# Performance work log

Measured on AMD Instinct MI355X. Metric: run time of the kernel, lower is better.

The kernel has to match this reference:

```python
import jax, jax.numpy as jnp
import numpy as np

NUM_HEADS = 8
CHUNK = 64          # dialtion / chunck_size
EPS = 1e-5          # InstanceNorm1d eps
NEG = -1e9


def setup_inputs() -> dict:
    key = jax.random.key(0)
    ks = jax.random.split(key, 8)
    N, C, T = 4, 512, 4096
    x = jax.random.normal(ks[0], (N, C, T), dtype=jnp.float32)
    q = jax.random.normal(ks[1], (N, C, T), dtype=jnp.float32)
    k = jax.random.normal(ks[2], (N, C, T), dtype=jnp.float32)
    v = jax.random.normal(ks[3], (N, C, T), dtype=jnp.float32)
    masks = jnp.ones((N, 1, T), dtype=jnp.float32)
    s = 1.0 / np.sqrt(C)
    W_in = jax.random.normal(ks[4], (3 * C, C), dtype=jnp.float32) * s   # packed q/k/v in-proj
    b_in = jnp.zeros((3 * C,), dtype=jnp.float32)
    W_out = jax.random.normal(ks[5], (C, C), dtype=jnp.float32) * s     # out-proj
    b_out = jnp.zeros((C,), dtype=jnp.float32)
    return {"x": x, "q": q, "k": k, "v": v, "masks": masks,
            "W_in": W_in, "b_in": b_in, "W_out": W_out, "b_out": b_out}


def _chunk_attn(q, k, v, masks, W_in, b_in, W_out, b_out):
    # q,k,v: [N, C, T]; masks: [N, 1, T]
    N, C, T = q.shape
    H, Dh = NUM_HEADS, C // NUM_HEADS
    nc = T // CHUNK
    Wq, Wk, Wv = jnp.split(W_in, 3, axis=0)
    bq, bk, bv = jnp.split(b_in, 3, axis=0)

    def proj(t, W, b):
        # [N,C,T] -> chunked heads [N, nc, CHUNK, H, Dh]
        t = t.transpose(0, 2, 1) @ W.T + b            # [N, T, C]
        return t.reshape(N, nc, CHUNK, H, Dh)

    qh = proj(q, Wq, bq)
    kh = proj(k, Wk, bk)
    vh = proj(v, Wv, bv)

    scale = 1.0 / jnp.sqrt(jnp.asarray(Dh, q.dtype))
    # intra-chunk scores: [N, nc, H, CHUNK, CHUNK]
    scores = jnp.einsum('bnqhd,bnkhd->bnhqk', qh, kh) * scale
    km = masks[:, 0, :].reshape(N, nc, CHUNK)         # key validity per chunk
    scores = scores + jnp.where(km[:, :, None, None, :] > 0, 0.0, NEG)
    attn = jax.nn.softmax(scores, axis=-1)
    out = jnp.einsum('bnhqk,bnkhd->bnqhd', attn, vh).reshape(N, T, C)
    out = out @ W_out.T + b_out                        # [N, T, C]
    out = out.transpose(0, 2, 1) * masks               # [N, C, T], re-mask
    return out


def reference(x, q, k, v, masks, W_in, b_in, W_out, b_out):
    out = _chunk_attn(q, k, v, masks, W_in, b_in, W_out, b_out) + x
    # InstanceNorm1d (affine=False): normalize each (n, c) row over T
    mu = jnp.mean(out, axis=2, keepdims=True)
    var = jnp.mean(jnp.square(out - mu), axis=2, keepdims=True)
    return (out - mu) * jax.lax.rsqrt(var + EPS)
```

## Files before the change

### kernel.cpp

```cpp
#include <hip/hip_runtime.h>
#include <hip/hip_bf16.h>

#define NB 4
#define CC 512
#define TT 4096
#define C3 1536
#define CQK 1024
#define NTC (NB*TT*CC)

typedef __attribute__((ext_vector_type(4))) float f32x4;
typedef __attribute__((ext_vector_type(8))) short short8;
typedef unsigned short ushort;
typedef __attribute__((ext_vector_type(8))) ushort u16x8;

__device__ __forceinline__ ushort f2bf(float f){
    union { float f; unsigned u; } x; x.f = f;
    unsigned r = x.u + 0x7fffu + ((x.u >> 16) & 1u);
    return (ushort)(r >> 16);
}

__device__ __forceinline__ ushort2 pk2bf(float a, float b){
    float2 f2; f2.x = a; f2.y = b;
    __hip_bfloat162 h = __float22bfloat162_rn(f2);
    union { __hip_bfloat162 h2; ushort2 u2; } u; u.h2 = h;
    return u.u2;
}

__device__ __forceinline__ void gload16(const void* g, void* l){
    __builtin_amdgcn_global_load_lds((const __attribute__((address_space(1))) void*)g,
                                     (__attribute__((address_space(3))) void*)l,
                                     16, 0, 0);
}

__device__ __forceinline__ int apos(int m, int cb){
    return (m*8 + ((cb + m + (m >> 3)) & 7))*8;
}

__global__ __launch_bounds__(256) void wcvt(const float* __restrict__ Wi,
                                            const float* __restrict__ Wo,
                                            ushort* __restrict__ Wb,
                                            ushort* __restrict__ Wob){
    int idx0 = blockIdx.x * 1024 + threadIdx.x;
    for (int i = 0; i < 4; ++i){
        int idx = idx0 + i*256;
        const float* src; ushort* dst; int j;
        if (idx < 196608){ src = Wi; dst = Wb;  j = idx; }
        else             { src = Wo; dst = Wob; j = idx - 196608; }
        f32x4 vv = *((const f32x4*)src + j);
        ushort4 o;
        *(ushort2*)&o.x = pk2bf(vv[0], vv[1]);
        *(ushort2*)&o.z = pk2bf(vv[2], vv[3]);
        *((ushort4*)dst + j) = o;
    }
}

__global__ __launch_bounds__(256, 3) void proj_gemm(const float* __restrict__ q,
                                                    const float* __restrict__ k,
                                                    const float* __restrict__ v,
                                                    const ushort* __restrict__ Wb,
                                                    const float* __restrict__ b_in,
                                                    ushort* __restrict__ P,
                                                    ushort* __restrict__ Vt){
    __shared__ __align__(16) ushort smem[24576];
    ushort* sA  = smem;
    ushort* sB0 = smem + 8192;
    ushort* sB1 = smem + 16384;
    const int tid = threadIdx.x;
    const int bid = blockIdx.x;
    const int mtile  = ((bid & 7) << 4) | ((bid >> 3) & 15);
    const int cotile = bid >> 7;
    const int co0 = cotile * 128;
    const int m0  = mtile * 128;
    const int which = co0 >> 9;
    const float* src = (which == 0) ? q : (which == 1) ? k : v;
    const int n  = m0 >> 12, t0 = m0 & 4095;
    const ushort* Bbase = Wb + (size_t)co0*CC;
    const int w = tid >> 6, lane = tid & 63;
    const int wr = w >> 1, wc = w & 1;
    const int l15 = lane & 15, quad = lane >> 4;
    const int hlf = lane >> 5, tq = lane & 31;

    const int mrB = tid >> 3;
    const int kkB = (tid & 7) ^ (mrB & 7);
    const ushort* gB0 = Bbase + (size_t)mrB*CC + kkB*8;
    const int lB0 = (tid & ~63) * 8;

    const float* Ab = src + (size_t)n*CC*TT + t0 + tq*4;
    const int ce0 = w*16 + hlf*2;

    f32x4 a0[4], a1[4];
    #pragma unroll
    for (int u = 0; u < 4; ++u){
        a0[u] = *(const f32x4*)(Ab + (size_t)(ce0 + u*4    )*TT);
        a1[u] = *(const f32x4*)(Ab + (size_t)(ce0 + u*4 + 1)*TT);
    }
    #pragma unroll
    for (int i = 0; i < 4; ++i)
        gload16(gB0 + (size_t)i*32*CC, sB0 + lB0 + i*2048);
    #pragma unroll
    for (int u = 0; u < 4; ++u){
        int ce = ce0 + u*4;
        int cb = ce >> 3, off = ce & 7;
        #pragma unroll
        for (int j = 0; j < 4; ++j)
            *(ushort2*)&sA[apos(tq*4 + j, cb) + off] = pk2bf(a0[u][j], a1[u][j]);
    }
    __syncthreads();

    f32x4 acc[4][4] = {};
    for (int kb = 0; kb < 8; ++kb){
        ushort* sBc = (kb & 1) ? sB1 : sB0;
        ushort* sBn = (kb & 1) ? sB0 : sB1;
        if (kb < 7){
            const float* Abn = Ab + (size_t)((kb+1)*64)*TT;
            #pragma unroll
            for (int u = 0; u < 4; ++u){
                a0[u] = *(const f32x4*)(Abn + (size_t)(ce0 + u*4    )*TT);
                a1[u] = *(const f32x4*)(Abn + (size_t)(ce0 + u*4 + 1)*TT);
            }
            #pragma unroll
            for (int i = 0; i < 4; ++i)
                gload16(gB0 + (size_t)i*32*CC + (kb+1)*64, sBn + lB0 + i*2048);
        }
        #pragma unroll
        for (int ks = 0; ks < 2; ++ks){
            short8 aF[4], bF[4];
            #pragma unroll
            for (int mi = 0; mi < 4; ++mi){
                int m = wr*64 + mi*16 + l15;
                aF[mi] = *(const short8*)&sA[apos(m, ks*4 + quad)];
            }
            #pragma unroll
            for (int ni = 0; ni < 4; ++ni){
                int m = wc*64 + ni*16 + l15;
                bF[ni] = *(const short8*)&sBc[(m*8 + ((ks*4 + quad) ^ (m & 7)))*8];
            }
            #pragma unroll
            for (int mi = 0; mi < 4; ++mi)
                #pragma unroll
                for (int ni = 0; ni < 4; ++ni)
                    acc[mi][ni] = __builtin_amdgcn_mfma_f32_16x16x32_bf16(
                        aF[mi], bF[ni], acc[mi][ni], 0, 0, 0);
        }
        __syncthreads();
        if (kb < 7){
            #pragma unroll
            for (int u = 0; u < 4; ++u){
                int ce = ce0 + u*4;
                int cb = ce >> 3, off = ce & 7;
                #pragma unroll
                for (int j = 0; j < 4; ++j)
                    *(ushort2*)&sA[apos(tq*4 + j, cb) + off] = pk2bf(a0[u][j], a1[u][j]);
            }
        }
        __syncthreads();
    }

    float bj[4];
    for (int ni = 0; ni < 4; ++ni) bj[ni] = b_in[co0 + wc*64 + ni*16 + l15];

    __syncthreads();
    ushort* sOut = smem;
    if (which < 2){
        for (int mi = 0; mi < 4; ++mi){
            int mrow = wr*64 + mi*16 + quad*4;
            for (int ni = 0; ni < 4; ++ni){
                int col = wc*64 + ni*16 + l15;
                for (int r = 0; r < 4; ++r)
                    sOut[(mrow + r)*136 + col] = f2bf(acc[mi][ni][r] + bj[ni]);
            }
        }
    } else {
        for (int mi = 0; mi < 4; ++mi){
            int mrow = wr*64 + mi*16 + quad*4;
            for (int ni = 0; ni < 4; ++ni){
                int col = wc*64 + ni*16 + l15;
                ushort4 o4;
                o4.x = f2bf(acc[mi][ni][0] + bj[ni]);
                o4.y = f2bf(acc[mi][ni][1] + bj[ni]);
                o4.z = f2bf(acc[mi][ni][2] + bj[ni]);
                o4.w = f2bf(acc[mi][ni][3] + bj[ni]);
                *(ushort4*)&sOut[col*136 + mrow] = o4;
            }
        }
    }
    __syncthreads();
    if (which < 2){
        for (int i = 0; i < 8; ++i){
            int flat = i*256 + tid;
            int row = flat >> 4, cs = (flat & 15)*8;
            u16x8 val = *(const u16x8*)&sOut[row*136 + cs];
            *(u16x8*)(P + (size_t)(m0 + row)*CQK + which*512 + (co0 & 511) + cs) = val;
        }
    } else {
        for (int i = 0; i < 8; ++i){
            int flat = i*256 + tid;
            int row = flat >> 4, cs = (flat & 15)*8;
            int cl = (co0 - 1024) + row;
            int h = cl >> 6, d = cl & 63;
            u16x8 val = *(const u16x8*)&sOut[row*136 + cs];
            *(u16x8*)(Vt + (((size_t)n*8 + h)*64 + d)*TT + t0 + cs) = val;
        }
    }
}

__global__ __launch_bounds__(256) void attn_kernel(const ushort* __restrict__ P,
                                                   const ushort* __restrict__ Vt,
                                                   const float* __restrict__ masks,
                                                   ushort* __restrict__ ctx){
    __shared__ __align__(16) ushort sQ[64*64], sK[64*64], sV[64*64];
    __shared__ __align__(16) ushort sP[64][72];
    __shared__ __align__(16) ushort sO[64*72];
    int bid = blockIdx.x;
    int h = bid & 7, ch = (bid >> 3) & 63, n = bid >> 9;
    const int tid = threadIdx.x, lane = tid & 63, w = tid >> 6;
    const int l15 = lane & 15, quad = lane >> 4;
    const size_t rowbase = (size_t)n*TT + (size_t)ch*64;
    for (int i = 0; i < 2; ++i){
        int slot = i*256 + tid;
        int r = slot >> 3, k8 = slot & 7, kk = k8 ^ (r & 7);
        int lbase = (i*256 + (tid & ~63)) * 8;
        const ushort* gq = P + (rowbase + r)*CQK + h*64 + kk*8;
        gload16(gq,        sQ + lbase);
        gload16(gq + 512,  sK + lbase);
        const ushort* gv = Vt + (((size_t)n*8 + h)*64 + r)*TT + ch*64 + kk*8;
        gload16(gv,        sV + lbase);
    }
    __syncthreads();
    const int m0w = w*16;
    short8 aQ[2]; f32x4 accS[4] = {};
    for (int ks = 0; ks < 2; ++ks){
        int m = m0w + l15;
        aQ[ks] = *(const short8*)&sQ[(m*8 + ((ks*4 + quad) ^ (m & 7)))*8];
    }
    for (int ni = 0; ni < 4; ++ni)
        for (int ks = 0; ks < 2; ++ks){
            int m = ni*16 + l15;
            short8 bK = *(const short8*)&sK[(m*8 + ((ks*4 + quad) ^ (m & 7)))*8];
            accS[ni] = __builtin_amdgcn_mfma_f32_16x16x32_bf16(aQ[ks], bK, accS[ni], 0,0,0);
        }
    float madd[4];
    for (int ni = 0; ni < 4; ++ni){
        float mv = masks[(size_t)n*TT + ch*64 + ni*16 + l15];
        madd[ni] = (mv > 0.f) ? 0.f : -1e9f;
    }
    float s[4][4];
    for (int ni = 0; ni < 4; ++ni)
        for (int r = 0; r < 4; ++r) s[ni][r] = accS[ni][r]*0.125f + madd[ni];
    float ex[4][4];
    for (int r = 0; r < 4; ++r){
        float m1 = fmaxf(fmaxf(s[0][r], s[1][r]), fmaxf(s[2][r], s[3][r]));
        for (int d = 1; d < 16; d <<= 1) m1 = fmaxf(m1, __shfl_xor(m1, d));
        float a = 0.f;
        for (int ni = 0; ni < 4; ++ni){ float e = __expf(s[ni][r] - m1); ex[ni][r] = e; a += e; }
        for (int d = 1; d < 16; d <<= 1) a += __shfl_xor(a, d);
        float rs = 1.0f / a;
        for (int ni = 0; ni < 4; ++ni)
            sP[m0w + quad*4 + r][ni*16 + l15] = f2bf(ex[ni][r] * rs);
    }
    short8 aP[2]; f32x4 accO[4] = {};
    for (int ks = 0; ks < 2; ++ks)
        aP[ks] = *(const short8*)&sP[m0w + l15][ks*32 + quad*8];
    for (int ni = 0; ni < 4; ++ni)
        for (int ks = 0; ks < 2; ++ks){
            int m = ni*16 + l15;
            short8 bV = *(const short8*)&sV[(m*8 + ((ks*4 + quad) ^ (m & 7)))*8];
            accO[ni] = __builtin_amdgcn_mfma_f32_16x16x32_bf16(aP[ks], bV, accO[ni], 0,0,0);
        }
    for (int ni = 0; ni < 4; ++ni)
        for (int r = 0; r < 4; ++r)
            sO[(m0w + quad*4 + r)*72 + ni*16 + l15] = f2bf(accO[ni][r]);
    __syncthreads();
    for (int i = 0; i < 2; ++i){
        int flat = i*256 + tid;
        int row = flat >> 3, cs = (flat & 7)*8;
        u16x8 val = *(const u16x8*)&sO[row*72 + cs];
        *(u16x8*)(ctx + (rowbase + row)*CC + h*64 + cs) = val;
    }
}

__global__ __launch_bounds__(256) void out_gemm(const ushort* __restrict__ ctx,
                                                const ushort* __restrict__ Wob,
                                                const float* __restrict__ b_out,
                                                const float* __restrict__ x,
                                                const float* __restrict__ masks,
                                                float* __restrict__ out){
    __shared__ __align__(16) ushort smem[24576];
    ushort* sA0 = smem;
    ushort* sA1 = smem + 8192;
    ushort* sB0 = smem + 16384;
    ushort* sB1 = smem + 20480;
    float* fOut = (float*)smem;
    const int tid = threadIdx.x;
    const int bid = blockIdx.x;
    const int mtile  = ((bid & 7) << 4) | ((bid >> 3) & 15);
    const int cotile = bid >> 7;
    const int co0 = cotile * 64;
    const int m0  = mtile * 128;
    const int n = m0 >> 12, t0 = m0 & 4095;
    const ushort* Abase = ctx + (size_t)m0*CC;
    const ushort* Bbase = Wob + (size_t)co0*CC;
    const int w = tid >> 6, lane = tid & 63;
    const int wr = w >> 1, wc = w & 1;
    const int l15 = lane & 15, quad = lane >> 4;

    const int mr = tid >> 3;
    const int kk = (tid & 7) ^ (mr & 7);
    const ushort* gA0 = Abase + (size_t)mr*CC + kk*8;
    const ushort* gB0 = Bbase + (size_t)mr*CC + kk*8;
    const int lS = (tid & ~63) * 8;

    #pragma unroll
    for (int i = 0; i < 4; ++i) gload16(gA0 + (size_t)i*32*CC, sA0 + lS + i*2048);
    #pragma unroll
    for (int i = 0; i < 2; ++i) gload16(gB0 + (size_t)i*32*CC, sB0 + lS + i*2048);

    f32x4 acc[4][2] = {};
    for (int kb = 0; kb < 8; ++kb){
        ushort* sAc = (kb & 1) ? sA1 : sA0;
        ushort* sBc = (kb & 1) ? sB1 : sB0;
        ushort* sAn = (kb & 1) ? sA0 : sA1;
        ushort* sBn = (kb & 1) ? sB0 : sB1;
        __syncthreads();
        if (kb < 7){
            #pragma unroll
            for (int i = 0; i < 4; ++i)
                gload16(gA0 + (size_t)i*32*CC + (kb+1)*64, sAn + lS + i*2048);
            #pragma unroll
            for (int i = 0; i < 2; ++i)
                gload16(gB0 + (size_t)i*32*CC + (kb+1)*64, sBn + lS + i*2048);
        }
        #pragma unroll
        for (int ks = 0; ks < 2; ++ks){
            short8 aF[4], bF[2];
            #pragma unroll
            for (int mi = 0; mi < 4; ++mi){
                int m = wr*64 + mi*16 + l15;
                aF[mi] = *(const short8*)&sAc[(m*8 + ((ks*4 + quad) ^ (m & 7)))*8];
            }
            #pragma unroll
            for (int ni = 0; ni < 2; ++ni){
                int m = wc*32 + ni*16 + l15;
                bF[ni] = *(const short8*)&sBc[(m*8 + ((ks*4 + quad) ^ (m & 7)))*8];
            }
            #pragma unroll
            for (int mi = 0; mi < 4; ++mi)
                #pragma unroll
                for (int ni = 0; ni < 2; ++ni)
                    acc[mi][ni] = __builtin_amdgcn_mfma_f32_16x16x32_bf16(
                        aF[mi], bF[ni], acc[mi][ni], 0, 0, 0);
        }
    }
    float bo[2];
    for (int ni = 0; ni < 2; ++ni) bo[ni] = b_out[co0 + wc*32 + ni*16 + l15];

    __syncthreads();
    for (int mi = 0; mi < 4; ++mi){
        int tl = wr*64 + mi*16 + quad*4;
        for (int ni = 0; ni < 2; ++ni){
            int cl = wc*32 + ni*16 + l15;
            f32x4 vv;
            for (int r = 0; r < 4; ++r) vv[r] = acc[mi][ni][r] + bo[ni];
            *(f32x4*)&fOut[cl*132 + tl] = vv;
        }
    }
    __syncthreads();
    for (int i = 0; i < 8; ++i){
        int flat = i*256 + tid;
        int co = flat >> 5, ts = (flat & 31)*4;
        f32x4 a = *(const f32x4*)&fOut[co*132 + ts];
        f32x4 mk = *(const f32x4*)(masks + (size_t)n*TT + t0 + ts);
        f32x4 xv = *(const f32x4*)(x + ((size_t)n*CC + co0 + co)*TT + t0 + ts);
        f32x4 o;
        for (int r = 0; r < 4; ++r) o[r] = a[r]*mk[r] + xv[r];
        *(f32x4*)(out + ((size_t)n*CC + co0 + co)*TT + t0 + ts) = o;
    }
}

__global__ __launch_bounds__(256) void inorm(float* __restrict__ out){
    __shared__ float sS[4], sQ2[4];
    float* row = out + (size_t)blockIdx.x * TT;
    f32x4 vbuf[4];
    float s = 0.f, ss = 0.f;
    for (int i = 0; i < 4; ++i){
        f32x4 vv = *(const f32x4*)(row + (size_t)(i*256 + threadIdx.x)*4);
        vbuf[i] = vv;
        for (int r = 0; r < 4; ++r){ s += vv[r]; ss += vv[r]*vv[r]; }
    }
    for (int d = 1; d < 64; d <<= 1){ s += __shfl_xor(s, d); ss += __shfl_xor(ss, d); }
    int w = threadIdx.x >> 6;
    if ((threadIdx.x & 63) == 0){ sS[w] = s; sQ2[w] = ss; }
    __syncthreads();
    s  = sS[0] + sS[1] + sS[2] + sS[3];
    ss = sQ2[0] + sQ2[1] + sQ2[2] + sQ2[3];
    float mean = s * (1.0f/TT);
    float var  = ss * (1.0f/TT) - mean*mean;
    float rstd = rsqrtf(var + 1e-5f);
    for (int i = 0; i < 4; ++i){
        f32x4 vv = vbuf[i], o;
        for (int r = 0; r < 4; ++r) o[r] = (vv[r] - mean) * rstd;
        *(f32x4*)(row + (size_t)(i*256 + threadIdx.x)*4) = o;
    }
}

extern "C" void kernel_launch(void* const* d_in, const int* in_sizes, int n_in,
                              void* d_out, int out_size, void* d_ws, size_t ws_size,
                              hipStream_t stream) {
    const float* x     = (const float*)d_in[0];
    const float* q     = (const float*)d_in[1];
    const float* k     = (const float*)d_in[2];
    const float* v     = (const float*)d_in[3];
    const float* masks = (const float*)d_in[4];
    const float* W_in  = (const float*)d_in[5];
    const float* b_in  = (const float*)d_in[6];
    const float* W_out = (const float*)d_in[7];
    const float* b_out = (const float*)d_in[8];
    float* out = (float*)d_out;

    ushort* ws  = (ushort*)d_ws;
    ushort* ctx = ws;
    ushort* Wb  = ws + (size_t)NTC;
    ushort* Wob = Wb + 786432;
    ushort* P   = Wob + 262144;
    ushort* Vt  = P + (size_t)NB*TT*CQK;

    wcvt<<<256, 256, 0, stream>>>(W_in, W_out, Wb, Wob);
    proj_gemm<<<1536, 256, 0, stream>>>(q, k, v, Wb, b_in, P, Vt);
    attn_kernel<<<2048, 256, 0, stream>>>(P, Vt, masks, ctx);
    out_gemm<<<1024, 256, 0, stream>>>(ctx, Wob, b_out, x, masks, out);
    inorm<<<2048, 256, 0, stream>>>(out);
}
```

Measured before the change: 243.0 us.

## Fuse chunk attention with output projection in one kernel

Merges the attention kernel and the output-projection GEMM into a single kernel. Each 512-thread block handles one 64-token chunk across all 8 heads, with two 256-thread groups working on alternating heads and double-buffered async Q/K/V staging. Per-head context tiles stay in LDS and are multiplied immediately against W_out, which is read directly from global memory without LDS staging, so the bf16 ctx buffer no longer makes a round trip through HBM. The cost is a grid of only 256 blocks, a large register-resident 64x64 accumulator per wave, and explicit barriers and waitcnts, which may reduce occupancy and latency hiding.

```diff
diff --git a/kernel.cpp b/kernel.cpp
--- a/kernel.cpp
+++ b/kernel.cpp
@@ -12,6 +12,11 @@
 typedef __attribute__((ext_vector_type(8))) short short8;
 typedef unsigned short ushort;
 typedef __attribute__((ext_vector_type(8))) ushort u16x8;
+
+#define SBAR()  __builtin_amdgcn_s_barrier()
+#define SCHED0() __builtin_amdgcn_sched_barrier(0)
+#define WAITV(n) asm volatile("s_waitcnt vmcnt(" #n ")" ::: "memory")
+#define WAITLG() asm volatile("s_waitcnt lgkmcnt(0)" ::: "memory")
 
 __device__ __forceinline__ ushort f2bf(float f){
     union { float f; unsigned u; } x; x.f = f;
@@ -204,176 +209,164 @@
     }
 }
 
-__global__ __launch_bounds__(256) void attn_kernel(const ushort* __restrict__ P,
+__global__ __launch_bounds__(512, 2) void attn_out(const ushort* __restrict__ P,
                                                    const ushort* __restrict__ Vt,
+                                                   const ushort* __restrict__ Wob,
+                                                   const float* __restrict__ b_out,
+                                                   const float* __restrict__ x,
                                                    const float* __restrict__ masks,
-                                                   ushort* __restrict__ ctx){
-    __shared__ __align__(16) ushort sQ[64*64], sK[64*64], sV[64*64];
-    __shared__ __align__(16) ushort sP[64][72];
-    __shared__ __align__(16) ushort sO[64*72];
-    int bid = blockIdx.x;
-    int h = bid & 7, ch = (bid >> 3) & 63, n = bid >> 9;
+                                                   float* __restrict__ out){
+    __shared__ __align__(16) ushort sS[49152];
+    __shared__ __align__(16) ushort sPP[2*64*72];
+    __shared__ __align__(16) ushort sOO[2*64*72];
+    const int bid = blockIdx.x;
+    const int ch = bid & 63, n = bid >> 6;
     const int tid = threadIdx.x, lane = tid & 63, w = tid >> 6;
+    const int g = w >> 2, wg = w & 3;
     const int l15 = lane & 15, quad = lane >> 4;
     const size_t rowbase = (size_t)n*TT + (size_t)ch*64;
-    for (int i = 0; i < 2; ++i){
-        int slot = i*256 + tid;
-        int r = slot >> 3, k8 = slot & 7, kk = k8 ^ (r & 7);
-        int lbase = (i*256 + (tid & ~63)) * 8;
-        const ushort* gq = P + (rowbase + r)*CQK + h*64 + kk*8;
-        gload16(gq,        sQ + lbase);
-        gload16(gq + 512,  sK + lbase);
-        const ushort* gv = Vt + (((size_t)n*8 + h)*64 + r)*TT + ch*64 + kk*8;
-        gload16(gv,        sV + lbase);
-    }
-    __syncthreads();
-    const int m0w = w*16;
-    short8 aQ[2]; f32x4 accS[4] = {};
-    for (int ks = 0; ks < 2; ++ks){
-        int m = m0w + l15;
-        aQ[ks] = *(const short8*)&sQ[(m*8 + ((ks*4 + quad) ^ (m & 7)))*8];
-    }
-    for (int ni = 0; ni < 4; ++ni)
-        for (int ks = 0; ks < 2; ++ks){
-            int m = ni*16 + l15;
-            short8 bK = *(const short8*)&sK[(m*8 + ((ks*4 + quad) ^ (m & 7)))*8];
-            accS[ni] = __builtin_amdgcn_mfma_f32_16x16x32_bf16(aQ[ks], bK, accS[ni], 0,0,0);
-        }
+    const int tidg = tid & 255;
+    const int r0s = tidg >> 3;
+    const int lb0 = (tidg & ~63) * 8;
+
+#define SBUF(b) (sS + (b)*24576 + g*12288)
+
+#define STAGE(h, b) do{                                                        \
+    ushort* _sq = SBUF(b);                                                     \
+    _Pragma("unroll")                                                          \
+    for (int i = 0; i < 2; ++i){                                               \
+        int r = r0s + i*32;                                                    \
+        int kk = (tidg & 7) ^ (r & 7);                                         \
+        int lbase = lb0 + i*2048;                                              \
+        const ushort* gq = P + (rowbase + r)*CQK + (h)*64 + kk*8;              \
+        gload16(gq,        _sq + lbase);                                       \
+        gload16(gq + 512,  _sq + 4096 + lbase);                                \
+        const ushort* gv = Vt + (((size_t)n*8 + (h))*64 + r)*TT + ch*64 + kk*8;\
+        gload16(gv,        _sq + 8192 + lbase);                                \
+    } }while(0)
+
+    const int m0w = wg*16;
+    ushort* sP = sPP + g*4608;
+    ushort* sO = sOO + g*4608;
+
+    const int co0w = w*64;
+    const ushort* Wp = Wob + (size_t)(co0w + l15)*CC + quad*8;
+    f32x4 acc[4][4] = {};
+
     float madd[4];
+    #pragma unroll
     for (int ni = 0; ni < 4; ++ni){
         float mv = masks[(size_t)n*TT + ch*64 + ni*16 + l15];
         madd[ni] = (mv > 0.f) ? 0.f : -1e9f;
     }
-    float s[4][4];
-    for (int ni = 0; ni < 4; ++ni)
-        for (int r = 0; r < 4; ++r) s[ni][r] = accS[ni][r]*0.125f + madd[ni];
-    float ex[4][4];
-    for (int r = 0; r < 4; ++r){
-        float m1 = fmaxf(fmaxf(s[0][r], s[1][r]), fmaxf(s[2][r], s[3][r]));
-        for (int d = 1; d < 16; d <<= 1) m1 = fmaxf(m1, __shfl_xor(m1, d));
-        float a = 0.f;
-        for (int ni = 0; ni < 4; ++ni){ float e = __expf(s[ni][r] - m1); ex[ni][r] = e; a += e; }
-        for (int d = 1; d < 16; d <<= 1) a += __shfl_xor(a, d);
-        float rs = 1.0f / a;
-        for (int ni = 0; ni < 4; ++ni)
-            sP[m0w + quad*4 + r][ni*16 + l15] = f2bf(ex[ni][r] * rs);
-    }
-    short8 aP[2]; f32x4 accO[4] = {};
-    for (int ks = 0; ks < 2; ++ks)
-        aP[ks] = *(const short8*)&sP[m0w + l15][ks*32 + quad*8];
-    for (int ni = 0; ni < 4; ++ni)
-        for (int ks = 0; ks < 2; ++ks){
-            int m = ni*16 + l15;
-            short8 bV = *(const short8*)&sV[(m*8 + ((ks*4 + quad) ^ (m & 7)))*8];
-            accO[ni] = __builtin_amdgcn_mfma_f32_16x16x32_bf16(aP[ks], bV, accO[ni], 0,0,0);
-        }
-    for (int ni = 0; ni < 4; ++ni)
-        for (int r = 0; r < 4; ++r)
-            sO[(m0w + quad*4 + r)*72 + ni*16 + l15] = f2bf(accO[ni][r]);
-    __syncthreads();
-    for (int i = 0; i < 2; ++i){
-        int flat = i*256 + tid;
-        int row = flat >> 3, cs = (flat & 7)*8;
-        u16x8 val = *(const u16x8*)&sO[row*72 + cs];
-        *(u16x8*)(ctx + (rowbase + row)*CC + h*64 + cs) = val;
-    }
-}
-
-__global__ __launch_bounds__(256) void out_gemm(const ushort* __restrict__ ctx,
-                                                const ushort* __restrict__ Wob,
-                                                const float* __restrict__ b_out,
-                                                const float* __restrict__ x,
-                                                const float* __restrict__ masks,
-                                                float* __restrict__ out){
-    __shared__ __align__(16) ushort smem[24576];
-    ushort* sA0 = smem;
-    ushort* sA1 = smem + 8192;
-    ushort* sB0 = smem + 16384;
-    ushort* sB1 = smem + 20480;
-    float* fOut = (float*)smem;
-    const int tid = threadIdx.x;
-    const int bid = blockIdx.x;
-    const int mtile  = ((bid & 7) << 4) | ((bid >> 3) & 15);
-    const int cotile = bid >> 7;
-    const int co0 = cotile * 64;
-    const int m0  = mtile * 128;
-    const int n = m0 >> 12, t0 = m0 & 4095;
-    const ushort* Abase = ctx + (size_t)m0*CC;
-    const ushort* Bbase = Wob + (size_t)co0*CC;
-    const int w = tid >> 6, lane = tid & 63;
-    const int wr = w >> 1, wc = w & 1;
-    const int l15 = lane & 15, quad = lane >> 4;
-
-    const int mr = tid >> 3;
-    const int kk = (tid & 7) ^ (mr & 7);
-    const ushort* gA0 = Abase + (size_t)mr*CC + kk*8;
-    const ushort* gB0 = Bbase + (size_t)mr*CC + kk*8;
-    const int lS = (tid & ~63) * 8;
-
-    #pragma unroll
-    for (int i = 0; i < 4; ++i) gload16(gA0 + (size_t)i*32*CC, sA0 + lS + i*2048);
-    #pragma unroll
-    for (int i = 0; i < 2; ++i) gload16(gB0 + (size_t)i*32*CC, sB0 + lS + i*2048);
-
-    f32x4 acc[4][2] = {};
-    for (int kb = 0; kb < 8; ++kb){
-        ushort* sAc = (kb & 1) ? sA1 : sA0;
-        ushort* sBc = (kb & 1) ? sB1 : sB0;
-        ushort* sAn = (kb & 1) ? sA0 : sA1;
-        ushort* sBn = (kb & 1) ? sB0 : sB1;
-        __syncthreads();
-        if (kb < 7){
-            #pragma unroll
-            for (int i = 0; i < 4; ++i)
-                gload16(gA0 + (size_t)i*32*CC + (kb+1)*64, sAn + lS + i*2048);
-            #pragma unroll
-            for (int i = 0; i < 2; ++i)
-                gload16(gB0 + (size_t)i*32*CC + (kb+1)*64, sBn + lS + i*2048);
-        }
+
+    STAGE(g, 0);
+    for (int hp = 0; hp < 4; ++hp){
+        if (hp < 3) STAGE(2*(hp+1) + g, (hp+1)&1);
+        SCHED0();
+        if (hp < 3) { WAITV(6); } else { WAITV(0); }
+        SBAR();
+        SCHED0();
+        {
+            const ushort* sQ = SBUF(hp&1);
+            const ushort* sK = sQ + 4096;
+            const ushort* sV = sQ + 8192;
+            short8 aQ[2]; f32x4 accS[4] = {};
+            #pragma unroll
+            for (int ks = 0; ks < 2; ++ks){
+                int m = m0w + l15;
+                aQ[ks] = *(const short8*)&sQ[(m*8 + ((ks*4 + quad) ^ (m & 7)))*8];
+            }
+            #pragma unroll
+            for (int ni = 0; ni < 4; ++ni)
+                #pragma unroll
+                for (int ks = 0; ks < 2; ++ks){
+                    int m = ni*16 + l15;
+                    short8 bK = *(const short8*)&sK[(m*8 + ((ks*4 + quad) ^ (m & 7)))*8];
+                    accS[ni] = __builtin_amdgcn_mfma_f32_16x16x32_bf16(aQ[ks], bK, accS[ni], 0,0,0);
+                }
+            float s[4][4];
+            #pragma unroll
+            for (int ni = 0; ni < 4; ++ni)
+                #pragma unroll
+                for (int r = 0; r < 4; ++r) s[ni][r] = accS[ni][r]*0.125f + madd[ni];
+            #pragma unroll
+            for (int r = 0; r < 4; ++r){
+                float m1 = fmaxf(fmaxf(s[0][r], s[1][r]), fmaxf(s[2][r], s[3][r]));
+                for (int d = 1; d < 16; d <<= 1) m1 = fmaxf(m1, __shfl_xor(m1, d));
+                float ex[4]; float a = 0.f;
+                #pragma unroll
+                for (int ni = 0; ni < 4; ++ni){ float e = __expf(s[ni][r] - m1); ex[ni] = e; a += e; }
+                for (int d = 1; d < 16; d <<= 1) a += __shfl_xor(a, d);
+                float rs = 1.0f / a;
+                #pragma unroll
+                for (int ni = 0; ni < 4; ++ni)
+                    sP[(m0w + quad*4 + r)*72 + ni*16 + l15] = f2bf(ex[ni] * rs);
+            }
+            short8 aP[2]; f32x4 accO[4] = {};
+            #pragma unroll
+            for (int ks = 0; ks < 2; ++ks)
+                aP[ks] = *(const short8*)&sP[(m0w + l15)*72 + ks*32 + quad*8];
+            #pragma unroll
+            for (int ni = 0; ni < 4; ++ni)
+                #pragma unroll
+                for (int ks = 0; ks < 2; ++ks){
+                    int m = ni*16 + l15;
+                    short8 bV = *(const short8*)&sV[(m*8 + ((ks*4 + quad) ^ (m & 7)))*8];
+                    accO[ni] = __builtin_amdgcn_mfma_f32_16x16x32_bf16(aP[ks], bV, accO[ni], 0,0,0);
+                }
+            #pragma unroll
+            for (int ni = 0; ni < 4; ++ni)
+                #pragma unroll
+                for (int r = 0; r < 4; ++r)
+                    sO[(m0w + quad*4 + r)*72 + ni*16 + l15] = f2bf(accO[ni][r]);
+        }
+        WAITLG();
+        SBAR();
+        SCHED0();
         #pragma unroll
-        for (int ks = 0; ks < 2; ++ks){
-            short8 aF[4], bF[2];
-            #pragma unroll
-            for (int mi = 0; mi < 4; ++mi){
-                int m = wr*64 + mi*16 + l15;
-                aF[mi] = *(const short8*)&sAc[(m*8 + ((ks*4 + quad) ^ (m & 7)))*8];
-            }
-            #pragma unroll
-            for (int ni = 0; ni < 2; ++ni){
-                int m = wc*32 + ni*16 + l15;
-                bF[ni] = *(const short8*)&sBc[(m*8 + ((ks*4 + quad) ^ (m & 7)))*8];
-            }
-            #pragma unroll
-            for (int mi = 0; mi < 4; ++mi)
-                #pragma unroll
-                for (int ni = 0; ni < 2; ++ni)
-                    acc[mi][ni] = __builtin_amdgcn_mfma_f32_16x16x32_bf16(
-                        aF[mi], bF[ni], acc[mi][ni], 0, 0, 0);
-        }
-    }
-    float bo[2];
-    for (int ni = 0; ni < 2; ++ni) bo[ni] = b_out[co0 + wc*32 + ni*16 + l15];
-
-    __syncthreads();
+        for (int g2 = 0; g2 < 2; ++g2){
+            const ushort* sOg = sOO + g2*4608;
+            #pragma unroll
+            for (int ks = 0; ks < 2; ++ks){
+                const int c0 = hp*128 + g2*64 + ks*32;
+                short8 aF[4];
+                #pragma unroll
+                for (int mi = 0; mi < 4; ++mi)
+                    aF[mi] = *(const short8*)&sOg[(mi*16 + l15)*72 + ks*32 + quad*8];
+                #pragma unroll
+                for (int ni = 0; ni < 4; ++ni){
+                    short8 bF = *(const short8*)(Wp + (size_t)(ni*16)*CC + c0);
+                    #pragma unroll
+                    for (int mi = 0; mi < 4; ++mi)
+                        acc[mi][ni] = __builtin_amdgcn_mfma_f32_16x16x32_bf16(
+                            aF[mi], bF, acc[mi][ni], 0, 0, 0);
+                }
+            }
+        }
+    }
+#undef STAGE
+#undef SBUF
+
+    float bo[4];
+    #pragma unroll
+    for (int ni = 0; ni < 4; ++ni) bo[ni] = b_out[co0w + ni*16 + l15];
+    #pragma unroll
     for (int mi = 0; mi < 4; ++mi){
-        int tl = wr*64 + mi*16 + quad*4;
-        for (int ni = 0; ni < 2; ++ni){
-            int cl = wc*32 + ni*16 + l15;
-            f32x4 vv;
-            for (int r = 0; r < 4; ++r) vv[r] = acc[mi][ni][r] + bo[ni];
-            *(f32x4*)&fOut[cl*132 + tl] = vv;
-        }
-    }
-    __syncthreads();
-    for (int i = 0; i < 8; ++i){
-        int flat = i*256 + tid;
-        int co = flat >> 5, ts = (flat & 31)*4;
-        f32x4 a = *(const f32x4*)&fOut[co*132 + ts];
-        f32x4 mk = *(const f32x4*)(masks + (size_t)n*TT + t0 + ts);
-        f32x4 xv = *(const f32x4*)(x + ((size_t)n*CC + co0 + co)*TT + t0 + ts);
-        f32x4 o;
-        for (int r = 0; r < 4; ++r) o[r] = a[r]*mk[r] + xv[r];
-        *(f32x4*)(out + ((size_t)n*CC + co0 + co)*TT + t0 + ts) = o;
+        int tl = mi*16 + quad*4;
+        size_t tg = (size_t)ch*64 + tl;
+        f32x4 mk = *(const f32x4*)(masks + (size_t)n*TT + tg);
+        #pragma unroll
+        for (int ni = 0; ni < 4; ++ni){
+            int co = co0w + ni*16 + l15;
+            const float* xp = x + ((size_t)n*CC + co)*TT + tg;
+            f32x4 xv = *(const f32x4*)xp;
+            f32x4 o;
+            #pragma unroll
+            for (int r = 0; r < 4; ++r)
+                o[r] = (acc[mi][ni][r] + bo[ni])*mk[r] + xv[r];
+            *(f32x4*)(out + ((size_t)n*CC + co)*TT + tg) = o;
+        }
     }
 }
 
@@ -418,7 +411,6 @@
     float* out = (float*)d_out;
 
     ushort* ws  = (ushort*)d_ws;
-    ushort* ctx = ws;
     ushort* Wb  = ws + (size_t)NTC;
     ushort* Wob = Wb + 786432;
     ushort* P   = Wob + 262144;
@@ -426,7 +418,6 @@
 
     wcvt<<<256, 256, 0, stream>>>(W_in, W_out, Wb, Wob);
     proj_gemm<<<1536, 256, 0, stream>>>(q, k, v, Wb, b_in, P, Vt);
-    attn_kernel<<<2048, 256, 0, stream>>>(P, Vt, masks, ctx);
-    out_gemm<<<1024, 256, 0, stream>>>(ctx, Wob, b_out, x, masks, out);
+    attn_out<<<256, 512, 0, stream>>>(P, Vt, Wob, b_out, x, masks, out);
     inorm<<<2048, 256, 0, stream>>>(out);
 }
```

New measurement: 248.1 us. +2.1%, slower.
